# Kernel optimization log

Hardware: AMD Instinct MI355X
Metric: run time of the kernel (lower is better)

## Reference

```python
import jax, jax.numpy as jnp
import numpy as np

VOCAB = 50257
CUTOFF = (10000, 50000, 50257)  # cutoff + [vocab_size] per __init__
D = 1024
B, T = 2, 1024
HEAD_SZ = CUTOFF[0] + 2  # cutoff[0] + n_tail_clusters


def setup_inputs() -> dict:
    key = jax.random.key(0)
    ks = jax.random.split(key, 7)
    def xavier(k, shp):
        # xavier_uniform as in init_weights
        bound = np.sqrt(6.0 / (shp[0] + shp[1])).astype(np.float32)
        return jax.random.uniform(k, shp, dtype=jnp.float32, minval=-bound, maxval=bound)
    return {
        "input": jax.random.normal(ks[0], (B, T, D), dtype=jnp.float32),
        "target": jax.random.randint(ks[1], (B, T), 0, VOCAB),
        "head_w": xavier(ks[2], (HEAD_SZ, D)),              # [10002, 1024]
        "t0_a": xavier(ks[3], (D, D)),                       # [1024, 1024]
        "t0_b": xavier(ks[4], (CUTOFF[1] - CUTOFF[0], D)),   # [40000, 1024]
        "t1_a": xavier(ks[5], (D // 4, D)),                  # [256, 1024]
        "t1_b": xavier(ks[6], (CUTOFF[2] - CUTOFF[1], D // 4)),  # [207, 256]
    }


def reference(input, target, head_w, t0_a, t0_b, t1_a, t1_b):
    # Faithful jax version of AdaptiveSoftmax.get_log_prob (eval mode, dropout=0).
    # Torch updates log_probs[idxs, start:end] only for rows whose target lies in
    # cluster i (leaving other rows zero); we express the same gather->small GEMM
    # chain->log_softmax->prior-add->scatter via masked writes (jit-friendly).
    bsz, length, dim = input.shape
    xi = input.reshape(-1, dim)                     # [N, D]
    tgt = target.reshape(-1)                        # [N]

    head_lp = jax.nn.log_softmax(xi @ head_w.T, axis=1)        # [N, HEAD_SZ]
    tail_priors = head_lp[:, CUTOFF[0] - 1:HEAD_SZ - 1]        # [N, 2]

    log_probs = jnp.zeros((xi.shape[0], VOCAB), dtype=input.dtype)
    log_probs = log_probs.at[:, :HEAD_SZ].set(head_lp)

    tails = ((t0_a, t0_b), (t1_a, t1_b))
    for i, (wa, wb) in enumerate(tails):
        lo, hi = CUTOFF[i], CUTOFF[i + 1]
        mask = (tgt >= lo) & (tgt < hi)                        # [N]
        # Linear(D, D//4**i) -> Linear(D//4**i, hi-lo), then log_softmax + prior
        tail_lp = jax.nn.log_softmax((xi @ wa.T) @ wb.T, axis=1) + tail_priors[:, i:i + 1]
        log_probs = log_probs.at[:, lo:hi].set(
            jnp.where(mask[:, None], tail_lp, log_probs[:, lo:hi]))
    return log_probs.reshape(bsz, length, VOCAB)
```

## Files before the change

kernel.cpp:

```cpp
#include <hip/hip_runtime.h>

typedef unsigned short u16;
typedef unsigned int u32;
typedef __attribute__((ext_vector_type(4))) float f32x4;
typedef __bf16 bf16x8 __attribute__((ext_vector_type(8)));
typedef __attribute__((ext_vector_type(8))) unsigned short u16x8;

__device__ __forceinline__ u16 f2bf(float x) {
    u32 u = __builtin_bit_cast(u32, x);
    u += 0x7FFFu + ((u >> 16) & 1u);
    return (u16)(u >> 16);
}
__device__ __forceinline__ float bf2f(u16 u) {
    return __builtin_bit_cast(float, ((u32)u) << 16);
}
__device__ __forceinline__ void gld_lds16(void* lds, const void* g) {
    __builtin_amdgcn_global_load_lds(
        (const __attribute__((address_space(1))) void*)g,
        (__attribute__((address_space(3))) void*)lds, 16, 0, 0);
}

__device__ __forceinline__ size_t pack_base_tail(long row) {
    return (size_t)row * 100514 + 59936 - ((row * 2) & 7);
}
__device__ __forceinline__ size_t pack_base_head(long row) {
    return (size_t)row * 100514 + 20480 - ((row * 2) & 7);
}

__global__ __launch_bounds__(256) void cvt_all(const float* __restrict__ x,
                                               const float* __restrict__ hw,
                                               const float* __restrict__ t0a,
                                               const float* __restrict__ t1a,
                                               const float* __restrict__ t0b,
                                               const float* __restrict__ t1b,
                                               u16* __restrict__ XI, u16* __restrict__ HW,
                                               u16* __restrict__ TAB, u16* __restrict__ T0B,
                                               u16* __restrict__ T1B) {
    int b = blockIdx.x;
    const float* src; u16* dst; int n, b0, nb;
    if (b < 80)        { src = x;    dst = XI;            n = 2097152;  b0 = 0;    nb = 80;   }
    else if (b < 472)  { src = hw;   dst = HW;            n = 10242048; b0 = 80;   nb = 392;  }
    else if (b < 512)  { src = t0a;  dst = TAB;           n = 1048576;  b0 = 472;  nb = 40;   }
    else if (b < 522)  { src = t1a;  dst = TAB + 1048576; n = 262144;   b0 = 512;  nb = 10;   }
    else if (b < 2086) { src = t0b;  dst = T0B;           n = 40960000; b0 = 522;  nb = 1564; }
    else if (b < 2090) { src = t1b;  dst = T1B;           n = 65792;    b0 = 2086; nb = 4;    }
    else if (b < 2100) { src = 0;    dst = HW + 10242048; n = 243712;   b0 = 2090; nb = 10;   }
    else               { src = 0;    dst = T0B + 40960000; n = 196608;  b0 = 2100; nb = 8;    }
    int i0 = (b - b0) * 1024 + threadIdx.x * 4;
    int stride = nb * 1024;
    if (src) {
        for (int i = i0; i < n; i += stride) {
            float4 v = *(const float4*)(src + i);
            ushort4 o;
            o.x = f2bf(v.x); o.y = f2bf(v.y); o.z = f2bf(v.z); o.w = f2bf(v.w);
            *(ushort4*)(dst + i) = o;
        }
    } else {
        ushort4 z = {0, 0, 0, 0};
        for (int i = i0; i < n; i += stride) *(ushort4*)(dst + i) = z;
    }
}

__global__ __launch_bounds__(256) void build_map(const int* __restrict__ tgt,
                                                 int* __restrict__ rowlist,
                                                 int* __restrict__ cntbuf) {
    __shared__ int cs[257];
    int t = threadIdx.x;
    int cnt_local = 0;
    int mk[8];
#pragma unroll
    for (int k = 0; k < 8; k++) {
        int tg = tgt[t * 8 + k];
        mk[k] = (tg >= 10000 && tg < 50000) ? 1 : 0;
        cnt_local += mk[k];
    }
    cs[t + 1] = cnt_local;
    __syncthreads();
    if (t == 0) {
        cs[0] = 0;
        for (int i = 1; i <= 256; i++) cs[i] += cs[i - 1];
        cntbuf[0] = cs[256];
        cntbuf[1] = (cs[256] + 255) & ~255;
    }
    __syncthreads();
    int cnt = cs[256];
    int offm = cs[t];
    int offu = cnt + (t * 8 - cs[t]);
#pragma unroll
    for (int k = 0; k < 8; k++) {
        if (mk[k]) rowlist[offm++] = t * 8 + k;
        else       rowlist[offu++] = t * 8 + k;
    }
}

#define PH_BAR() do { __builtin_amdgcn_sched_barrier(0); __builtin_amdgcn_s_barrier(); __builtin_amdgcn_sched_barrier(0); } while (0)

template <int TAIL>
__global__ __launch_bounds__(512, 2) void gemm256(const u16* __restrict__ A,
                                                  const u16* __restrict__ B,
                                                  u16* __restrict__ outpk,
                                                  const int* __restrict__ rowlist,
                                                  const int* __restrict__ cntbuf,
                                                  float* __restrict__ part) {
    const int m0 = blockIdx.x * 256, n0 = blockIdx.y * 256;
    if (TAIL) { if (m0 >= cntbuf[1]) return; }
    __shared__ u16 lds[4][16384];
    const int tid = threadIdx.x;
    const int lane = tid & 63, wv = tid >> 6;
    const int wm = wv >> 2, wn = wv & 3;
    const int lr = lane & 15, hi = lane >> 4;

    const int c0 = tid, c1 = 512 + tid;
    int ga0 = m0 + ((c0 >> 6) << 4) + (c0 & 15);
    int ga1 = m0 + ((c1 >> 6) << 4) + (c1 & 15);
    const u16* sA0;
    const u16* sA1;
    if (TAIL) {
        sA0 = A + (size_t)rowlist[ga0] * 1280 + ((c0 >> 4) & 3) * 8;
        sA1 = A + (size_t)rowlist[ga1] * 1280 + ((c1 >> 4) & 3) * 8;
    } else {
        sA0 = A + (size_t)ga0 * 1024 + ((c0 >> 4) & 3) * 8;
        sA1 = A + (size_t)ga1 * 1024 + ((c1 >> 4) & 3) * 8;
    }
    const u16* sB0 = B + (size_t)(n0 + ((c0 >> 6) << 4) + (c0 & 15)) * 1024 + ((c0 >> 4) & 3) * 8;
    const u16* sB1 = B + (size_t)(n0 + ((c1 >> 6) << 4) + (c1 & 15)) * 1024 + ((c1 >> 4) & 3) * 8;

    f32x4 acc[8][4] = {};
    bf16x8 Bf[4], Af[4];

    auto stageA = [&](int buf, int kt) {
        char* d = (char*)&lds[buf][0] + tid * 16;
        gld_lds16(d,        sA0 + kt);
        gld_lds16(d + 8192, sA1 + kt);
    };
    auto stageB = [&](int buf, int kt) {
        char* d = (char*)&lds[buf][0] + tid * 16;
        gld_lds16(d + 16384, sB0 + kt);
        gld_lds16(d + 24576, sB1 + kt);
    };
    auto readB = [&](const u16* L) {
#pragma unroll
        for (int j = 0; j < 4; j++)
            Bf[j] = *(const bf16x8*)(L + 8192 + (wn * 4 + j) * 512 + hi * 128 + lr * 8);
    };
    auto readA = [&](const u16* L, int q) {
#pragma unroll
        for (int m = 0; m < 4; m++)
            Af[m] = *(const bf16x8*)(L + (wm * 8 + q * 4 + m) * 512 + hi * 128 + lr * 8);
    };
    auto mfma16 = [&](int q) {
        __builtin_amdgcn_s_setprio(1);
#pragma unroll
        for (int m = 0; m < 4; m++)
#pragma unroll
            for (int j = 0; j < 4; j++)
                acc[q * 4 + m][j] = __builtin_amdgcn_mfma_f32_16x16x32_bf16(Af[m], Bf[j], acc[q * 4 + m][j], 0, 0, 0);
        __builtin_amdgcn_s_setprio(0);
    };

    stageA(0, 0);  stageB(0, 0);
    stageA(1, 32); stageB(1, 32);
    asm volatile("s_waitcnt vmcnt(4)" ::: "memory");
    __builtin_amdgcn_s_barrier();
    __builtin_amdgcn_sched_barrier(0);

#pragma unroll 1
    for (int t = 0; t < 30; ++t) {
        const u16* L = &lds[t & 3][0];
        const int b2 = (t + 2) & 3, kt2 = (t + 2) * 32;
        readB(L); readA(L, 0);
        stageA(b2, kt2);
        PH_BAR();
        mfma16(0);
        PH_BAR();
        readA(L, 1);
        stageB(b2, kt2);
        asm volatile("s_waitcnt vmcnt(4)" ::: "memory");
        PH_BAR();
        mfma16(1);
        PH_BAR();
    }
    {
        const u16* L = &lds[2][0];
        readB(L); readA(L, 0);
        PH_BAR();
        mfma16(0);
        PH_BAR();
        readA(L, 1);
        asm volatile("s_waitcnt vmcnt(0)" ::: "memory");
        PH_BAR();
        mfma16(1);
        PH_BAR();
    }
    {
        const u16* L = &lds[3][0];
        readB(L); readA(L, 0);
        PH_BAR();
        mfma16(0);
        PH_BAR();
        readA(L, 1);
        __builtin_amdgcn_sched_barrier(0);
        mfma16(1);
    }

    const int cr = hi * 4, cc = lr;
    const int climit = TAIL ? 40000 : 10002;
    const int pstride = TAIL ? 628 : 160;
#pragma unroll
    for (int m = 0; m < 8; m++) {
#pragma unroll
        for (int q = 0; q < 4; q++) {
            int r = m0 + wm * 128 + m * 16 + cr + q;
            long orow = TAIL ? rowlist[r] : r;
            size_t base = TAIL ? pack_base_tail(orow) : pack_base_head(orow);
            u16* dst = outpk + base + n0 + wn * 64 + cc;
            float s = 0.f;
#pragma unroll
            for (int j = 0; j < 4; j++) {
                float v = acc[m][j][q];
                dst[j * 16] = f2bf(v);
                int col = n0 + wn * 64 + j * 16 + cc;
                s += (col < climit) ? __expf(v) : 0.f;
            }
            s += __shfl_xor(s, 1); s += __shfl_xor(s, 2);
            s += __shfl_xor(s, 4); s += __shfl_xor(s, 8);
            if (cc == 0) part[(size_t)r * pstride + (n0 >> 6) + wn] = s;
        }
    }
}

__global__ __launch_bounds__(256) void gemm_nt_bf16(const u16* __restrict__ A, int lda,
                                                    const u16* __restrict__ B, int ldb,
                                                    u16* __restrict__ Cb, long ldc, int K) {
    __shared__ u16 lA[128 * 32];
    __shared__ u16 lB[128 * 32];
    const int tid = threadIdx.x;
    const int lane = tid & 63, wv = tid >> 6;
    const int m0 = blockIdx.x * 128, n0 = blockIdx.y * 128;

    const u16* gA0 = A + (size_t)(m0 + (tid >> 2)) * lda + (tid & 3) * 8;
    const u16* gB0 = B + (size_t)(n0 + (tid >> 2)) * ldb + (tid & 3) * 8;
    char* dA = (char*)lA + wv * 1024;
    char* dB = (char*)lB + wv * 1024;

    f32x4 acc[4][4] = {};
    const int wm = wv >> 1, wn = wv & 1;
    const int lr = lane & 15;
    const int lk = (lane >> 4) * 8;

    for (int kt = 0; kt < K; kt += 32) {
        __syncthreads();
        gld_lds16(dA, gA0);
        gld_lds16(dA + 4096, gA0 + 64 * (size_t)lda);
        gld_lds16(dB, gB0);
        gld_lds16(dB + 4096, gB0 + 64 * (size_t)ldb);
        gA0 += 32; gB0 += 32;
        __syncthreads();

        bf16x8 af[4], bfr[4];
#pragma unroll
        for (int i = 0; i < 4; i++) {
            af[i]  = *(const bf16x8*)(lA + (wm * 64 + i * 16 + lr) * 32 + lk);
            bfr[i] = *(const bf16x8*)(lB + (wn * 64 + i * 16 + lr) * 32 + lk);
        }
#pragma unroll
        for (int i = 0; i < 4; i++)
#pragma unroll
            for (int j = 0; j < 4; j++)
                acc[i][j] = __builtin_amdgcn_mfma_f32_16x16x32_bf16(af[i], bfr[j], acc[i][j], 0, 0, 0);
    }

    const int cr = (lane >> 4) * 4;
    const int cc = lane & 15;
#pragma unroll
    for (int i = 0; i < 4; i++) {
        int rbase = m0 + wm * 64 + i * 16 + cr;
#pragma unroll
        for (int j = 0; j < 4; j++) {
            int c = n0 + wn * 64 + j * 16 + cc;
#pragma unroll
            for (int q = 0; q < 4; q++)
                Cb[(size_t)(rbase + q) * (size_t)ldc + c] = f2bf(acc[i][j][q]);
        }
    }
}

__global__ __launch_bounds__(256) void head_norm(float* __restrict__ out,
                                                 float* __restrict__ stats,
                                                 const float* __restrict__ parth) {
    const int row = blockIdx.x, tid = threadIdx.x;
    float s = (tid < 160) ? parth[(size_t)row * 160 + tid] : 0.f;
#pragma unroll
    for (int o = 32; o; o >>= 1) s += __shfl_xor(s, o);
    __shared__ float red[4];
    if ((tid & 63) == 0) red[tid >> 6] = s;
    __syncthreads();
    float logZ = __logf(red[0] + red[1] + red[2] + red[3]);
    const u16* pk = (const u16*)out + pack_base_head(row);
    float* p = out + (size_t)row * 50257;
    for (int k = 0; k < 5; k++) {
        int c0 = k * 2048 + tid * 8;
        if (c0 + 8 <= 10002) {
            u16x8 xv = *(const u16x8*)(pk + c0);
#pragma unroll
            for (int z = 0; z < 8; z++) p[c0 + z] = bf2f(xv[z]) - logZ;
        } else if (c0 < 10002) {
            for (int z = 0; c0 + z < 10002; z++) p[c0 + z] = bf2f(pk[c0 + z]) - logZ;
        }
    }
    if (tid == 0) {
        float* st = stats + row * 8;
        float l0 = bf2f(pk[9999]) - logZ;
        float l1 = bf2f(pk[10000]) - logZ;
        float l2 = bf2f(pk[10001]) - logZ;
        st[0] = l0; st[1] = l1; st[2] = l1; st[3] = l2;
    }
}

__global__ __launch_bounds__(256) void tail0_norm(float* __restrict__ out,
                                                  const int* __restrict__ rowlist,
                                                  const int* __restrict__ cntbuf,
                                                  const float* __restrict__ ST,
                                                  const float* __restrict__ PART) {
    const int b = blockIdx.x, tid = threadIdx.x;
    const int cnt = cntbuf[0];
    const long row = rowlist[b];
    float* p = out + (size_t)row * 50257 + 10000;
    __shared__ float red[4];
    if (b < cnt) {
        float s = 0.f;
        for (int c = tid; c < 628; c += 256) s += PART[(size_t)b * 628 + c];
#pragma unroll
        for (int o = 32; o; o >>= 1) s += __shfl_xor(s, o);
        if ((tid & 63) == 0) red[tid >> 6] = s;
        __syncthreads();
        float Aa = __logf(red[0] + red[1] + red[2] + red[3]) - ST[row * 8 + 0];
        const u16* src = (const u16*)out + pack_base_tail(row);
        for (int k = 0; k < 5; k++) {
            float v[4][8];
#pragma unroll
            for (int g = 0; g < 4; g++) {
                int o = 2048 * g + tid * 8;
                if (o < 8000) {
                    u16x8 xv = *(const u16x8*)(src + 8000 * k + o);
#pragma unroll
                    for (int z = 0; z < 8; z++) v[g][z] = bf2f(xv[z]);
                }
            }
            __syncthreads();
#pragma unroll
            for (int g = 0; g < 4; g++) {
                int o = 2048 * g + tid * 8;
                if (o < 8000) {
                    int e = 8000 * k + o;
#pragma unroll
                    for (int z = 0; z < 8; z++) p[e + z] = v[g][z] - Aa;
                }
            }
            __syncthreads();
        }
    } else {
        float v0 = ST[row * 8 + 2], v1 = ST[row * 8 + 3];
        for (int e = tid; e < 40000; e += 256) p[e] = 0.f;
        if (tid == 0) { p[0] = v0; p[1] = v1; }
    }
}

__global__ __launch_bounds__(256) void tail1_kernel(float* __restrict__ out,
                                                    const int* __restrict__ tgt,
                                                    const u16* __restrict__ proj,
                                                    const u16* __restrict__ t1b,
                                                    const float* __restrict__ stats) {
    const int row = blockIdx.x, tid = threadIdx.x;
    float* p = out + (size_t)row * 50257 + 50000;
    int t = tgt[row];
    if (t < 50000) {
        for (int c = tid; c < 257; c += 256) p[c] = 0.f;
        return;
    }
    __shared__ float pr[256];
    __shared__ float lg[257];
    __shared__ float red[4];
    pr[tid] = bf2f(proj[(size_t)row * 1280 + 1024 + tid]);
    __syncthreads();
    for (int c = tid; c < 257; c += 256) {
        const u16* w = t1b + c * 256;
        float acc = 0.f;
        for (int k = 0; k < 256; k++) acc += bf2f(w[k]) * pr[k];
        lg[c] = acc;
    }
    __syncthreads();
    float s = 0.f;
    for (int c = tid; c < 257; c += 256) s += __expf(lg[c]);
#pragma unroll
    for (int o = 32; o; o >>= 1) s += __shfl_xor(s, o);
    if ((tid & 63) == 0) red[tid >> 6] = s;
    __syncthreads();
    float A = __logf(red[0] + red[1] + red[2] + red[3]) - stats[row * 8 + 1];
    for (int c = tid; c < 257; c += 256) p[c] = lg[c] - A;
}

#define OFF_XI    0UL
#define OFF_HEADW 4194304UL
#define OFF_TAB   25165824UL
#define OFF_T0B   27787264UL
#define OFF_T1B   110100480UL
#define OFF_PROJ  110232064UL
#define OFF_ST    115474944UL
#define OFF_PART  115540480UL
#define OFF_PARTH 120685056UL
#define OFF_MAP   121995776UL
#define OFF_CNT   122003968UL

extern "C" void kernel_launch(void* const* d_in, const int* in_sizes, int n_in,
                              void* d_out, int out_size, void* d_ws, size_t ws_size,
                              hipStream_t stream) {
    const float* x   = (const float*)d_in[0];
    const int*   tgt = (const int*)d_in[1];
    const float* hw  = (const float*)d_in[2];
    const float* t0a = (const float*)d_in[3];
    const float* t0b = (const float*)d_in[4];
    const float* t1a = (const float*)d_in[5];
    const float* t1b = (const float*)d_in[6];
    float* out = (float*)d_out;
    char* ws = (char*)d_ws;

    u16* XI     = (u16*)(ws + OFF_XI);
    u16* HW     = (u16*)(ws + OFF_HEADW);
    u16* TAB    = (u16*)(ws + OFF_TAB);
    u16* T0B    = (u16*)(ws + OFF_T0B);
    u16* T1B    = (u16*)(ws + OFF_T1B);
    u16* PROJ   = (u16*)(ws + OFF_PROJ);
    float* ST   = (float*)(ws + OFF_ST);
    float* PART = (float*)(ws + OFF_PART);
    float* PARTH = (float*)(ws + OFF_PARTH);
    int* MAP    = (int*)(ws + OFF_MAP);
    int* CNT    = (int*)(ws + OFF_CNT);

    cvt_all<<<2108, 256, 0, stream>>>(x, hw, t0a, t1a, t0b, t1b, XI, HW, TAB, T0B, T1B);

    build_map<<<1, 256, 0, stream>>>(tgt, MAP, CNT);

    gemm256<0><<<dim3(8, 40), 512, 0, stream>>>(XI, HW, (u16*)d_out, nullptr, nullptr, PARTH);

    head_norm<<<2048, 256, 0, stream>>>(out, ST, PARTH);

    gemm_nt_bf16<<<dim3(16, 10), 256, 0, stream>>>(XI, 1024, TAB, 1024, PROJ, 1280L, 1024);

    gemm256<1><<<dim3(8, 157), 512, 0, stream>>>(PROJ, T0B, (u16*)d_out, MAP, CNT, PART);

    tail0_norm<<<2048, 256, 0, stream>>>(out, MAP, CNT, ST, PART);

    tail1_kernel<<<2048, 256, 0, stream>>>(out, tgt, PROJ, T1B, ST);
}
```

Baseline: 577.4 us.

## Replace 256x256 pipelined GEMM with 128x256 single-buffer tiles and swizzled block order

Swaps the 256x256 tile GEMM, which used a four-buffer LDS pipeline with explicit phase barriers, for a 128x256 tile kernel. The new kernel uses one LDS buffer with a plain syncthreads loop, fewer accumulators and launch bounds allowing 4 blocks per CU. It also remaps block IDs to group blocks for better L2 reuse and pads the tail row count to 128 instead of 256. The aim is higher occupancy, less wasted padding work on the masked tail rows and better load balancing across CUs. The cost is losing explicit software pipelining, so global-to-LDS loads are no longer overlapped with MFMA within a block and each block reuses its tiles less.

```diff
diff --git a/kernel.cpp b/kernel.cpp
--- a/kernel.cpp
+++ b/kernel.cpp
@@ -80,7 +80,7 @@
         cs[0] = 0;
         for (int i = 1; i <= 256; i++) cs[i] += cs[i - 1];
         cntbuf[0] = cs[256];
-        cntbuf[1] = (cs[256] + 255) & ~255;
+        cntbuf[1] = (cs[256] + 127) & ~127;
     }
     __syncthreads();
     int cnt = cs[256];
@@ -93,124 +93,66 @@
     }
 }
 
-#define PH_BAR() do { __builtin_amdgcn_sched_barrier(0); __builtin_amdgcn_s_barrier(); __builtin_amdgcn_sched_barrier(0); } while (0)
-
 template <int TAIL>
-__global__ __launch_bounds__(512, 2) void gemm256(const u16* __restrict__ A,
+__global__ __launch_bounds__(512, 4) void gemm128(const u16* __restrict__ A,
                                                   const u16* __restrict__ B,
                                                   u16* __restrict__ outpk,
                                                   const int* __restrict__ rowlist,
                                                   const int* __restrict__ cntbuf,
                                                   float* __restrict__ part) {
-    const int m0 = blockIdx.x * 256, n0 = blockIdx.y * 256;
+    const int NB = TAIL ? 157 : 40;
+    const int nwg = 16 * NB;
+    const int l = blockIdx.y * 16 + blockIdx.x;
+    const int w = (l & 7) * (nwg >> 3) + (l >> 3);
+    const int mblk = w & 15, nblk = w >> 4;
+    const int m0 = mblk * 128, n0 = nblk * 256;
     if (TAIL) { if (m0 >= cntbuf[1]) return; }
-    __shared__ u16 lds[4][16384];
+    __shared__ u16 lds[12288];
     const int tid = threadIdx.x;
     const int lane = tid & 63, wv = tid >> 6;
     const int wm = wv >> 2, wn = wv & 3;
     const int lr = lane & 15, hi = lane >> 4;
 
-    const int c0 = tid, c1 = 512 + tid;
-    int ga0 = m0 + ((c0 >> 6) << 4) + (c0 & 15);
-    int ga1 = m0 + ((c1 >> 6) << 4) + (c1 & 15);
-    const u16* sA0;
-    const u16* sA1;
-    if (TAIL) {
-        sA0 = A + (size_t)rowlist[ga0] * 1280 + ((c0 >> 4) & 3) * 8;
-        sA1 = A + (size_t)rowlist[ga1] * 1280 + ((c1 >> 4) & 3) * 8;
-    } else {
-        sA0 = A + (size_t)ga0 * 1024 + ((c0 >> 4) & 3) * 8;
-        sA1 = A + (size_t)ga1 * 1024 + ((c1 >> 4) & 3) * 8;
-    }
-    const u16* sB0 = B + (size_t)(n0 + ((c0 >> 6) << 4) + (c0 & 15)) * 1024 + ((c0 >> 4) & 3) * 8;
+    const int ra = ((tid >> 6) << 4) + (tid & 15);
+    const int ka = ((tid >> 4) & 3) * 8;
+    const u16* sA = TAIL ? A + (size_t)rowlist[m0 + ra] * 1280 + ka
+                         : A + (size_t)(m0 + ra) * 1024 + ka;
+    const int c1 = tid + 512;
+    const u16* sB0 = B + (size_t)(n0 + ra) * 1024 + ka;
     const u16* sB1 = B + (size_t)(n0 + ((c1 >> 6) << 4) + (c1 & 15)) * 1024 + ((c1 >> 4) & 3) * 8;
 
-    f32x4 acc[8][4] = {};
-    bf16x8 Bf[4], Af[4];
-
-    auto stageA = [&](int buf, int kt) {
-        char* d = (char*)&lds[buf][0] + tid * 16;
-        gld_lds16(d,        sA0 + kt);
-        gld_lds16(d + 8192, sA1 + kt);
-    };
-    auto stageB = [&](int buf, int kt) {
-        char* d = (char*)&lds[buf][0] + tid * 16;
-        gld_lds16(d + 16384, sB0 + kt);
-        gld_lds16(d + 24576, sB1 + kt);
-    };
-    auto readB = [&](const u16* L) {
+    f32x4 acc[4][4] = {};
+
+#pragma unroll 1
+    for (int kt = 0; kt < 1024; kt += 32) {
+        __syncthreads();
+        char* d = (char*)lds + tid * 16;
+        gld_lds16(d,         sA + kt);
+        gld_lds16(d + 8192,  sB0 + kt);
+        gld_lds16(d + 16384, sB1 + kt);
+        __syncthreads();
+
+        bf16x8 Bf[4];
 #pragma unroll
         for (int j = 0; j < 4; j++)
-            Bf[j] = *(const bf16x8*)(L + 8192 + (wn * 4 + j) * 512 + hi * 128 + lr * 8);
-    };
-    auto readA = [&](const u16* L, int q) {
-#pragma unroll
-        for (int m = 0; m < 4; m++)
-            Af[m] = *(const bf16x8*)(L + (wm * 8 + q * 4 + m) * 512 + hi * 128 + lr * 8);
-    };
-    auto mfma16 = [&](int q) {
-        __builtin_amdgcn_s_setprio(1);
-#pragma unroll
-        for (int m = 0; m < 4; m++)
+            Bf[j] = *(const bf16x8*)(lds + 4096 + (wn * 4 + j) * 512 + hi * 128 + lr * 8);
+#pragma unroll
+        for (int m = 0; m < 4; m++) {
+            bf16x8 Af = *(const bf16x8*)(lds + (wm * 4 + m) * 512 + hi * 128 + lr * 8);
 #pragma unroll
             for (int j = 0; j < 4; j++)
-                acc[q * 4 + m][j] = __builtin_amdgcn_mfma_f32_16x16x32_bf16(Af[m], Bf[j], acc[q * 4 + m][j], 0, 0, 0);
-        __builtin_amdgcn_s_setprio(0);
-    };
-
-    stageA(0, 0);  stageB(0, 0);
-    stageA(1, 32); stageB(1, 32);
-    asm volatile("s_waitcnt vmcnt(4)" ::: "memory");
-    __builtin_amdgcn_s_barrier();
-    __builtin_amdgcn_sched_barrier(0);
-
-#pragma unroll 1
-    for (int t = 0; t < 30; ++t) {
-        const u16* L = &lds[t & 3][0];
-        const int b2 = (t + 2) & 3, kt2 = (t + 2) * 32;
-        readB(L); readA(L, 0);
-        stageA(b2, kt2);
-        PH_BAR();
-        mfma16(0);
-        PH_BAR();
-        readA(L, 1);
-        stageB(b2, kt2);
-        asm volatile("s_waitcnt vmcnt(4)" ::: "memory");
-        PH_BAR();
-        mfma16(1);
-        PH_BAR();
-    }
-    {
-        const u16* L = &lds[2][0];
-        readB(L); readA(L, 0);
-        PH_BAR();
-        mfma16(0);
-        PH_BAR();
-        readA(L, 1);
-        asm volatile("s_waitcnt vmcnt(0)" ::: "memory");
-        PH_BAR();
-        mfma16(1);
-        PH_BAR();
-    }
-    {
-        const u16* L = &lds[3][0];
-        readB(L); readA(L, 0);
-        PH_BAR();
-        mfma16(0);
-        PH_BAR();
-        readA(L, 1);
-        __builtin_amdgcn_sched_barrier(0);
-        mfma16(1);
+                acc[m][j] = __builtin_amdgcn_mfma_f32_16x16x32_bf16(Af, Bf[j], acc[m][j], 0, 0, 0);
+        }
     }
 
     const int cr = hi * 4, cc = lr;
     const int climit = TAIL ? 40000 : 10002;
     const int pstride = TAIL ? 628 : 160;
 #pragma unroll
-    for (int m = 0; m < 8; m++) {
+    for (int m = 0; m < 4; m++) {
 #pragma unroll
         for (int q = 0; q < 4; q++) {
-            int r = m0 + wm * 128 + m * 16 + cr + q;
+            int r = m0 + wm * 64 + m * 16 + cr + q;
             long orow = TAIL ? rowlist[r] : r;
             size_t base = TAIL ? pack_base_tail(orow) : pack_base_head(orow);
             u16* dst = outpk + base + n0 + wn * 64 + cc;
@@ -441,13 +383,13 @@
 
     build_map<<<1, 256, 0, stream>>>(tgt, MAP, CNT);
 
-    gemm256<0><<<dim3(8, 40), 512, 0, stream>>>(XI, HW, (u16*)d_out, nullptr, nullptr, PARTH);
+    gemm128<0><<<dim3(16, 40), 512, 0, stream>>>(XI, HW, (u16*)d_out, nullptr, nullptr, PARTH);
 
     head_norm<<<2048, 256, 0, stream>>>(out, ST, PARTH);
 
     gemm_nt_bf16<<<dim3(16, 10), 256, 0, stream>>>(XI, 1024, TAB, 1024, PROJ, 1280L, 1024);
 
-    gemm256<1><<<dim3(8, 157), 512, 0, stream>>>(PROJ, T0B, (u16*)d_out, MAP, CNT, PART);
+    gemm128<1><<<dim3(16, 157), 512, 0, stream>>>(PROJ, T0B, (u16*)d_out, MAP, CNT, PART);
 
     tail0_norm<<<2048, 256, 0, stream>>>(out, MAP, CNT, ST, PART);
 
```

New measurement: 646.8 us. +12.0%, slower.
